# Performance work log

Hardware: AMD Instinct MI355X
Metric: run time of the kernel (lower is better)

The kernel has to match this reference:

```python
import jax, jax.numpy as jnp
import numpy as np

B, T, D_IN, D_MODEL, K = 32, 2048, 512, 1024, 64


def setup_inputs() -> dict:
    key = jax.random.key(0)
    ks = jax.random.split(key, 13)

    def lin(k, fan_in, fan_out):
        kw, kb = jax.random.split(k)
        bound = 1.0 / np.sqrt(fan_in)
        W = jax.random.uniform(kw, (fan_in, fan_out), minval=-bound, maxval=bound, dtype=jnp.float32)
        b = jax.random.uniform(kb, (fan_out,), minval=-bound, maxval=bound, dtype=jnp.float32)
        return W, b

    x = jax.random.normal(ks[0], (B, T, D_IN), dtype=jnp.float32)
    W_theta, b_theta = lin(ks[1], D_IN, K)
    W_lam, b_lam = lin(ks[2], D_IN, D_MODEL)
    W_delt, b_delt = lin(ks[3], D_IN, D_MODEL)
    W_inp, b_inp = lin(ks[4], D_IN, D_MODEL)
    W_par, b_par = lin(ks[5], 2 * K, 2)
    W_add, b_add = lin(ks[6], D_MODEL, 1)
    return {
        "x": x,
        "W_theta": W_theta, "b_theta": b_theta,
        "W_lam": W_lam, "b_lam": b_lam,
        "W_delt": W_delt, "b_delt": b_delt,
        "W_inp": W_inp, "b_inp": b_inp,
        "W_par": W_par, "b_par": b_par,
        "W_add": W_add, "b_add": b_add,
    }


def _forward(x, W_theta, b_theta, W_lam, b_lam, W_delt, b_delt, W_inp, b_inp, W_par, b_par, W_add, b_add):
    # Rotation recurrence: g starts at (1, 0) and is multiplied by e^{i*th_t} each
    # step, so the final g is exactly e^{i * sum_t th_t} (angles compose additively).
    th = jnp.pi * (jnp.einsum('btd,dk->btk', x, W_theta) + b_theta)  # (B,T,K)
    ang = jnp.sum(th, axis=1)                                        # (B,K)
    g_feat = jnp.concatenate([jnp.cos(ang), jnp.sin(ang)], axis=-1)  # (B,2K)

    # SSM state recurrence: s_t = alpha_t * s_{t-1} + delt_t * inp_t
    lam = jax.nn.softplus(jnp.einsum('btd,dm->btm', x, W_lam) + b_lam)
    delt = jax.nn.softplus(jnp.einsum('btd,dm->btm', x, W_delt) + b_delt)
    inp = jnp.einsum('btd,dm->btm', x, W_inp) + b_inp
    alpha = jnp.exp(-delt * lam)          # (B,T,M)
    drive = delt * inp                    # (B,T,M)

    def step(s, ad):
        a, d = ad
        return a * s + d, None

    s0 = jnp.zeros((x.shape[0], W_lam.shape[1]), dtype=x.dtype)
    s, _ = jax.lax.scan(step, s0, (jnp.swapaxes(alpha, 0, 1), jnp.swapaxes(drive, 0, 1)))

    parity_logits = g_feat @ W_par + b_par  # (B,2)
    add_pred = s @ W_add + b_add            # (B,1)
    return parity_logits, add_pred


def reference(x, W_theta, b_theta, W_lam, b_lam, W_delt, b_delt, W_inp, b_inp, W_par, b_par, W_add, b_add):
    return _forward(x, W_theta, b_theta, W_lam, b_lam, W_delt, b_delt, W_inp, b_inp, W_par, b_par, W_add, b_add)
```

## Files before the change

### kernel.cpp

```cpp
#include <hip/hip_runtime.h>
#include <hip/hip_bf16.h>

#define B_   32
#define T_   2048
#define DIN  512
#define DM   1024
#define K_   64
#define BT   64
#define NC   (T_/BT)
#define MT   (DM/64)
#define LDSTR 68

typedef unsigned short u16;
typedef unsigned int   u32;

__device__ __forceinline__ float bf2f(u16 h) {
    return __uint_as_float(((u32)h) << 16);
}
__device__ __forceinline__ void bf2x2(u32 w, float& lo, float& hi) {
    lo = __uint_as_float(w << 16);
    hi = __uint_as_float(w & 0xffff0000u);
}
__device__ __forceinline__ u16 f2bf(float f) {
    u32 u = __float_as_uint(f);
    u += 0x7fffu + ((u >> 16) & 1u);
    return (u16)(u >> 16);
}
__device__ __forceinline__ float softplusf(float z) {
    return fmaxf(z, 0.0f) + log1pf(expf(-fabsf(z)));
}

template<bool BF16>
__device__ __forceinline__ float ld1(const void* p, size_t i) {
    if (BF16) return bf2f(((const u16*)p)[i]);
    else      return ((const float*)p)[i];
}
template<bool BF16>
__device__ __forceinline__ void ld2(const void* p, size_t i, float& a, float& b) {
    if (BF16) { u32 w = *(const u32*)((const u16*)p + i); bf2x2(w, a, b); }
    else      { float2 v = *(const float2*)((const float*)p + i); a = v.x; b = v.y; }
}
template<bool BF16>
__device__ __forceinline__ void ld8(const void* p, size_t i, float* a) {
    if (BF16) {
        uint4 v = *(const uint4*)((const u16*)p + i);
        bf2x2(v.x, a[0], a[1]); bf2x2(v.y, a[2], a[3]);
        bf2x2(v.z, a[4], a[5]); bf2x2(v.w, a[6], a[7]);
    } else {
        float4 v0 = *(const float4*)((const float*)p + i);
        float4 v1 = *(const float4*)((const float*)p + i + 4);
        a[0]=v0.x; a[1]=v0.y; a[2]=v0.z; a[3]=v0.w;
        a[4]=v1.x; a[5]=v1.y; a[6]=v1.z; a[7]=v1.w;
    }
}

__device__ __forceinline__ bool sniff_is_bf16(const void* xraw) {
    __shared__ int flag_s;
    if (threadIdx.x < 64) {
        u16 w = ((const u16*)xraw)[threadIdx.x];
        float av = fabsf(bf2f(w));
        bool plausible = (av == 0.0f) || (av >= 9.094947e-13f && av <= 64.0f);
        unsigned long long m = __ballot(plausible ? 1 : 0);
        if (threadIdx.x == 0) flag_s = (__popcll(m) >= 56) ? 1 : 0;
    }
    __syncthreads();
    return flag_s != 0;
}

__global__ __launch_bounds__(64) void zero_accum_kernel(const void* x, void* out) {
    bool isbf = sniff_is_bf16(x);
    float* outf = (float*)out;
    if (threadIdx.x < 32) {
        if (isbf) outf[threadIdx.x] = 0.0f;
        else      outf[64 + threadIdx.x] = 0.0f;
    }
}

typedef __attribute__((ext_vector_type(8)))  short bf16x8;
typedef __attribute__((ext_vector_type(16))) float f32x16;

#define TCH 128
#define NCH (T_/TCH)
#define A_OFF  0
#define W_OFF  16384
#define AL_OFF 0
#define DR_OFF 32768

#define WS_COL_FLOATS  16384
#define WS_W_OFF_F     16384
#define WS_W_PLANE_U32 (3*256*1024)
#define WS_WFRAG_OFF_B 65536ULL
#define WS_WFRAG_BYTES (16ULL*16*24*1024)
#define WS_XFRAG_OFF_B (WS_WFRAG_OFF_B + WS_WFRAG_BYTES)
#define WS_XFRAG_BYTES (32ULL*16*16*16*1024)
#define WS_FULL_BYTES  (WS_XFRAG_OFF_B + WS_XFRAG_BYTES)

#define KC  64
__global__ __launch_bounds__(256, 2) void fused_ssm_mfma_bf16(
    const void* __restrict__ x,
    const void* __restrict__ Wlam, const void* __restrict__ blam,
    const void* __restrict__ Wdelt, const void* __restrict__ bdelt,
    const void* __restrict__ Winp, const void* __restrict__ binp,
    const void* __restrict__ Wadd,
    void* __restrict__ out)
{
    __shared__ __align__(16) unsigned char LDS[65536];

    const int tid = threadIdx.x;

    {
        int* flag = (int*)LDS;
        if (tid < 64) {
            u16 w0 = ((const u16*)x)[tid];
            float av = fabsf(bf2f(w0));
            bool plausible = (av == 0.0f) || (av >= 9.094947e-13f && av <= 64.0f);
            unsigned long long m = __ballot(plausible ? 1 : 0);
            if (tid == 0) *flag = (__popcll(m) >= 56) ? 1 : 0;
        }
        __syncthreads();
        int isbf = *flag;
        __syncthreads();
        if (!isbf) return;
    }

    const int swz = (blockIdx.x & 7) * 64 + (blockIdx.x >> 3);
    const int mg  = swz & 15;
    const int b   = swz >> 4;
    const int m0  = mg * 64;

    const int lane = tid & 63;
    const int w    = tid >> 6;
    const int p    = w >> 1;
    const int h    = w & 1;
    const int lr   = lane & 31;
    const int lg   = lane >> 5;

    const int colg = m0 + h*32 + lr;
    const float bL = bf2f(((const u16*)blam )[colg]);
    const float bD = bf2f(((const u16*)bdelt)[colg]);
    const float bI = bf2f(((const u16*)binp )[colg]);

    float* alphaS = (float*)(LDS + AL_OFF);
    float* driveS = (float*)(LDS + DR_OFF);

    float scarry = 0.0f;

    #pragma unroll 1
    for (int c = 0; c < NCH; c++) {
        f32x16 aL0, aL1, aD0, aD1, aI0, aI1;
        #pragma unroll
        for (int r = 0; r < 16; r++) {
            aL0[r] = bL; aL1[r] = bL;
            aD0[r] = bD; aD1[r] = bD;
            aI0[r] = bI; aI1[r] = bI;
        }

        #pragma unroll 1
        for (int kc = 0; kc < DIN/KC; kc++) {
            {
                const int t_l  = tid >> 1;
                const int half = tid & 1;
                const u16* xp = (const u16*)x
                    + ((size_t)b*T_ + (size_t)c*TCH + t_l)*DIN + kc*KC + half*32;
                uint4 v[4];
                v[0] = *(const uint4*)(xp);
                v[1] = *(const uint4*)(xp + 8);
                v[2] = *(const uint4*)(xp + 16);
                v[3] = *(const uint4*)(xp + 24);
                const int tt = t_l >> 5, tr = t_l & 31;
                #pragma unroll
                for (int q = 0; q < 4; q++) {
                    const int o  = half*4 + q;
                    const int ks = o >> 1, g = o & 1;
                    *(uint4*)(LDS + A_OFF + ((tt*4 + ks) << 10) + ((g*32 + tr) << 4)) = v[q];
                }
            }
            #pragma unroll
            for (int i = 0; i < 6; i++) {
                const int f   = w + 4*i;
                const int nt  = f >> 2, ks = f & 3;
                const int hh  = (nt >= 3) ? 1 : 0;
                const int mat = nt - 3*hh;
                const u16* Wp = (const u16*)(mat == 0 ? Wlam : (mat == 1 ? Wdelt : Winp));
                const size_t base = (size_t)(kc*KC + ks*16 + lg*8)*DM + (size_t)(m0 + hh*32 + lr);
                u32 e0 = Wp[base        ];
                u32 e1 = Wp[base +   DM ];
                u32 e2 = Wp[base + 2*DM ];
                u32 e3 = Wp[base + 3*DM ];
                u32 e4 = Wp[base + 4*DM ];
                u32 e5 = Wp[base + 5*DM ];
                u32 e6 = Wp[base + 6*DM ];
                u32 e7 = Wp[base + 7*DM ];
                uint4 pk;
                pk.x = e0 | (e1 << 16);
                pk.y = e2 | (e3 << 16);
                pk.z = e4 | (e5 << 16);
                pk.w = e6 | (e7 << 16);
                *(uint4*)(LDS + W_OFF + (f << 10) + (lane << 4)) = pk;
            }
            __syncthreads();

            #pragma unroll
            for (int ks = 0; ks < 4; ks++) {
                bf16x8 a0 = *(const bf16x8*)(LDS + A_OFF + (((2*p    )*4 + ks) << 10) + (lane << 4));
                bf16x8 a1 = *(const bf16x8*)(LDS + A_OFF + (((2*p + 1)*4 + ks) << 10) + (lane << 4));
                bf16x8 vL = *(const bf16x8*)(LDS + W_OFF + (((h*3 + 0)*4 + ks) << 10) + (lane << 4));
                bf16x8 vD = *(const bf16x8*)(LDS + W_OFF + (((h*3 + 1)*4 + ks) << 10) + (lane << 4));
                bf16x8 vI = *(const bf16x8*)(LDS + W_OFF + (((h*3 + 2)*4 + ks) << 10) + (lane << 4));
                aL0 = __builtin_amdgcn_mfma_f32_32x32x16_bf16(a0, vL, aL0, 0, 0, 0);
                aL1 = __builtin_amdgcn_mfma_f32_32x32x16_bf16(a1, vL, aL1, 0, 0, 0);
                aD0 = __builtin_amdgcn_mfma_f32_32x32x16_bf16(a0, vD, aD0, 0, 0, 0);
                aD1 = __builtin_amdgcn_mfma_f32_32x32x16_bf16(a1, vD, aD1, 0, 0, 0);
                aI0 = __builtin_amdgcn_mfma_f32_32x32x16_bf16(a0, vI, aI0, 0, 0, 0);
                aI1 = __builtin_amdgcn_mfma_f32_32x32x16_bf16(a1, vI, aI1, 0, 0, 0);
            }
            __syncthreads();
        }

        #pragma unroll
        for (int tt2 = 0; tt2 < 2; tt2++) {
            #pragma unroll
            for (int r = 0; r < 16; r++) {
                const float zl = tt2 ? aL1[r] : aL0[r];
                const float zd = tt2 ? aD1[r] : aD0[r];
                const float zi = tt2 ? aI1[r] : aI0[r];
                const float lam = softplusf(zl);
                const float dl  = softplusf(zd);
                const float av  = expf(-dl * lam);
                const float dv  = dl * zi;
                const int t_loc = (2*p + tt2)*32 + (r & 3) + 8*(r >> 2) + 4*lg;
                const int m_loc = h*32 + lr;
                alphaS[t_loc*64 + m_loc] = av;
                driveS[t_loc*64 + m_loc] = dv;
            }
        }
        __syncthreads();

        if (tid < 64) {
            float s = scarry;
            #pragma unroll 8
            for (int t = 0; t < TCH; t++)
                s = fmaf(alphaS[t*64 + tid], s, driveS[t*64 + tid]);
            scarry = s;
        }
        __syncthreads();
    }

    if (tid < 64) {
        float partial = scarry * bf2f(((const u16*)Wadd)[m0 + tid]);
        #pragma unroll
        for (int off = 32; off > 0; off >>= 1)
            partial += __shfl_down(partial, off, 64);
        if (tid == 0)
            atomicAdd(&((float*)out)[b], partial);
    }
}

__global__ __launch_bounds__(256) void convert_w_kernel(
    const void* __restrict__ x,
    const void* __restrict__ Wlam, const void* __restrict__ Wdelt,
    const void* __restrict__ Winp, float* __restrict__ ws)
{
    if (sniff_is_bf16(x)) return;
    const int mat = blockIdx.x >> 8;
    const int kp  = blockIdx.x & 255;
    const float* Wp = (mat == 0) ? (const float*)Wlam
                    : (mat == 1) ? (const float*)Wdelt : (const float*)Winp;
    u32* whi = (u32*)(ws + WS_W_OFF_F);
    u32* wlo = whi + WS_W_PLANE_U32;
    const size_t ro = (size_t)(2*kp)*DM;
    const size_t wo = ((size_t)mat*256 + kp)*DM;
    #pragma unroll
    for (int mm = 0; mm < 4; mm++) {
        const int m = mm*256 + threadIdx.x;
        float a0 = Wp[ro + m];
        float a1 = Wp[ro + DM + m];
        u16 h0 = f2bf(a0), h1 = f2bf(a1);
        float l0 = a0 - bf2f(h0);
        float l1 = a1 - bf2f(h1);
        whi[wo + m] = (u32)h0 | ((u32)h1 << 16);
        wlo[wo + m] = (__float_as_uint(l0) >> 16) | (__float_as_uint(l1) & 0xffff0000u);
    }
}

__global__ __launch_bounds__(256) void convert_w_frag_kernel(
    const void* __restrict__ x,
    const void* __restrict__ Wlam, const void* __restrict__ Wdelt,
    const void* __restrict__ Winp, u32* __restrict__ wsw)
{
    if (sniff_is_bf16(x)) return;
    const int kc = blockIdx.x & 15;
    const int mg = blockIdx.x >> 4;
    const int m0 = mg*64;
    u32* dst = wsw + (size_t)(mg*16 + kc) * 6144;
    #pragma unroll
    for (int i = 0; i < 6; i++) {
        const int u = threadIdx.x + 256*i;
        const int f = u >> 6;
        const int l = u & 63;
        const int hl = f & 1, ks = (f >> 1) & 1, nt = f >> 2;
        const int hh = nt / 3, mat = nt % 3;
        const float* Wp = (mat == 0) ? (const float*)Wlam
                        : (mat == 1) ? (const float*)Wdelt : (const float*)Winp;
        const int lr = l & 31, lg = l >> 5;
        const int kp0 = kc*16 + ks*8 + lg*4;
        const int m = m0 + hh*32 + lr;
        u32 q4[4];
        #pragma unroll
        for (int q = 0; q < 4; q++) {
            float a0 = Wp[(size_t)(2*(kp0+q)    )*DM + m];
            float a1 = Wp[(size_t)(2*(kp0+q) + 1)*DM + m];
            u16 h0 = f2bf(a0), h1 = f2bf(a1);
            if (hl == 0) {
                q4[q] = (u32)h0 | ((u32)h1 << 16);
            } else {
                float l0 = a0 - bf2f(h0);
                float l1 = a1 - bf2f(h1);
                q4[q] = (__float_as_uint(l0) >> 16) | (__float_as_uint(l1) & 0xffff0000u);
            }
        }
        *(uint4*)(dst + f*256 + l*4) = make_uint4(q4[0], q4[1], q4[2], q4[3]);
    }
}

#define KC2 32
__global__ __launch_bounds__(256) void convert_x_kernel(
    const void* __restrict__ x, u32* __restrict__ wsx)
{
    if (sniff_is_bf16(x)) return;
    const int kc = blockIdx.x & 15;
    const int c  = (blockIdx.x >> 4) & 15;
    const int b  = blockIdx.x >> 8;
    const int tid = threadIdx.x;
    const int t_l  = tid >> 1;
    const int half = tid & 1;
    const float* xp = (const float*)x
        + ((size_t)b*T_ + (size_t)c*TCH + t_l)*DIN + kc*KC2 + half*16;
    float vv[16];
    *(float4*)(vv)      = *(const float4*)(xp);
    *(float4*)(vv + 4)  = *(const float4*)(xp + 4);
    *(float4*)(vv + 8)  = *(const float4*)(xp + 8);
    *(float4*)(vv + 12) = *(const float4*)(xp + 12);
    u32 hi[8], lo[8];
    #pragma unroll
    for (int q = 0; q < 8; q++) {
        const float a0 = vv[2*q], a1 = vv[2*q+1];
        const u16 h0 = f2bf(a0), h1 = f2bf(a1);
        hi[q] = (u32)h0 | ((u32)h1 << 16);
        const float l0 = a0 - bf2f(h0);
        const float l1 = a1 - bf2f(h1);
        lo[q] = (__float_as_uint(l0) >> 16) | (__float_as_uint(l1) & 0xffff0000u);
    }
    u32* dst = wsx + ((((size_t)b*16 + c)*16 + kc) << 12);
    const int tt = t_l >> 5, tr = t_l & 31;
    const int fb = (tt*2 + half)*2;
    *(uint4*)(dst + fb*256     + (0*32 + tr)*4) = make_uint4(hi[0],hi[1],hi[2],hi[3]);
    *(uint4*)(dst + fb*256     + (1*32 + tr)*4) = make_uint4(hi[4],hi[5],hi[6],hi[7]);
    *(uint4*)(dst + (fb+1)*256 + (0*32 + tr)*4) = make_uint4(lo[0],lo[1],lo[2],lo[3]);
    *(uint4*)(dst + (fb+1)*256 + (1*32 + tr)*4) = make_uint4(lo[4],lo[5],lo[6],lo[7]);
}

#define STG_B 40960
__global__ __launch_bounds__(256, 2) void fused_ssm_mfma_fp32_full(
    const void* __restrict__ x,
    const void* __restrict__ blam, const void* __restrict__ bdelt,
    const void* __restrict__ binp, const void* __restrict__ Wadd,
    const u32* __restrict__ wsw, const u32* __restrict__ wsx,
    void* __restrict__ out)
{
    __shared__ __align__(16) unsigned char LDS[2*STG_B];

    const int tid = threadIdx.x;

    {
        int* flag = (int*)LDS;
        if (tid < 64) {
            u16 w0 = ((const u16*)x)[tid];
            float av = fabsf(bf2f(w0));
            bool plausible = (av == 0.0f) || (av >= 9.094947e-13f && av <= 64.0f);
            unsigned long long m = __ballot(plausible ? 1 : 0);
            if (tid == 0) *flag = (__popcll(m) >= 56) ? 1 : 0;
        }
        __syncthreads();
        int isbf = *flag;
        __syncthreads();
        if (isbf) return;
    }

    const int swz = (blockIdx.x & 7) * 64 + (blockIdx.x >> 3);
    const int mg  = swz & 15;
    const int b   = swz >> 4;
    const int m0  = mg * 64;

    const int lane = tid & 63;
    const int w    = tid >> 6;
    const int p    = w >> 1;
    const int h    = w & 1;
    const int lr   = lane & 31;
    const int lg   = lane >> 5;

    const int colg = m0 + h*32 + lr;
    const float bL = ((const float*)blam )[colg];
    const float bD = ((const float*)bdelt)[colg];
    const float bI = ((const float*)binp )[colg];

    float* alphaS = (float*)(LDS + AL_OFF);
    float* driveS = (float*)(LDS + DR_OFF);

    float scarry = 0.0f;

    #pragma unroll 1
    for (int c = 0; c < NCH; c++) {
        f32x16 aL0, aL1, aD0, aD1, aI0, aI1;
        #pragma unroll
        for (int r = 0; r < 16; r++) {
            aL0[r] = bL; aL1[r] = bL;
            aD0[r] = bD; aD1[r] = bD;
            aI0[r] = bI; aI1[r] = bI;
        }

        {
            const u32* ga = wsx + ((((size_t)b*16 + c)*16 + 0) << 12);
            const u32* gw = wsw + (size_t)(mg*16 + 0)*6144;
            uint4 sa[4], sw[6];
            #pragma unroll
            for (int j = 0; j < 4; j++) sa[j] = *(const uint4*)(ga + ((size_t)tid + 256*j)*4);
            #pragma unroll
            for (int j = 0; j < 6; j++) sw[j] = *(const uint4*)(gw + ((size_t)tid + 256*j)*4);
            #pragma unroll
            for (int j = 0; j < 4; j++) *(uint4*)(LDS + ((tid + 256*j) << 4)) = sa[j];
            #pragma unroll
            for (int j = 0; j < 6; j++) *(uint4*)(LDS + 16384 + ((tid + 256*j) << 4)) = sw[j];
        }
        __syncthreads();

        #pragma unroll 1
        for (int kc = 0; kc < DIN/KC2; kc++) {
            unsigned char* cur = LDS + (kc & 1)*STG_B;

            if (kc < DIN/KC2 - 1) {
                unsigned char* nxt = LDS + ((kc + 1) & 1)*STG_B;
                const u32* ga = wsx + ((((size_t)b*16 + c)*16 + (kc+1)) << 12);
                const u32* gw = wsw + (size_t)(mg*16 + (kc+1))*6144;
                uint4 sa[4], sw[6];
                #pragma unroll
                for (int j = 0; j < 4; j++) sa[j] = *(const uint4*)(ga + ((size_t)tid + 256*j)*4);
                #pragma unroll
                for (int j = 0; j < 6; j++) sw[j] = *(const uint4*)(gw + ((size_t)tid + 256*j)*4);
                #pragma unroll
                for (int j = 0; j < 4; j++) *(uint4*)(nxt + ((tid + 256*j) << 4)) = sa[j];
                #pragma unroll
                for (int j = 0; j < 6; j++) *(uint4*)(nxt + 16384 + ((tid + 256*j) << 4)) = sw[j];
            }

            #pragma unroll
            for (int ks = 0; ks < 2; ks++) {
                const int fa0 = ((2*p    )*2 + ks)*2;
                const int fa1 = ((2*p + 1)*2 + ks)*2;
                const int fL  = ((h*3 + 0)*2 + ks)*2;
                const int fD  = ((h*3 + 1)*2 + ks)*2;
                const int fI  = ((h*3 + 2)*2 + ks)*2;
                bf16x8 a0h = *(const bf16x8*)(cur + (fa0     << 10) + (lane << 4));
                bf16x8 a0l = *(const bf16x8*)(cur + ((fa0+1) << 10) + (lane << 4));
                bf16x8 a1h = *(const bf16x8*)(cur + (fa1     << 10) + (lane << 4));
                bf16x8 a1l = *(const bf16x8*)(cur + ((fa1+1) << 10) + (lane << 4));
                bf16x8 vLh = *(const bf16x8*)(cur + 16384 + (fL      << 10) + (lane << 4));
                bf16x8 vLl = *(const bf16x8*)(cur + 16384 + ((fL+1)  << 10) + (lane << 4));
                bf16x8 vDh = *(const bf16x8*)(cur + 16384 + (fD      << 10) + (lane << 4));
                bf16x8 vDl = *(const bf16x8*)(cur + 16384 + ((fD+1)  << 10) + (lane << 4));
                bf16x8 vIh = *(const bf16x8*)(cur + 16384 + (fI      << 10) + (lane << 4));
                bf16x8 vIl = *(const bf16x8*)(cur + 16384 + ((fI+1)  << 10) + (lane << 4));
                aL0 = __builtin_amdgcn_mfma_f32_32x32x16_bf16(a0h, vLh, aL0, 0, 0, 0);
                aL0 = __builtin_amdgcn_mfma_f32_32x32x16_bf16(a0h, vLl, aL0, 0, 0, 0);
                aL0 = __builtin_amdgcn_mfma_f32_32x32x16_bf16(a0l, vLh, aL0, 0, 0, 0);
                aL1 = __builtin_amdgcn_mfma_f32_32x32x16_bf16(a1h, vLh, aL1, 0, 0, 0);
                aL1 = __builtin_amdgcn_mfma_f32_32x32x16_bf16(a1h, vLl, aL1, 0, 0, 0);
                aL1 = __builtin_amdgcn_mfma_f32_32x32x16_bf16(a1l, vLh, aL1, 0, 0, 0);
                aD0 = __builtin_amdgcn_mfma_f32_32x32x16_bf16(a0h, vDh, aD0, 0, 0, 0);
                aD0 = __builtin_amdgcn_mfma_f32_32x32x16_bf16(a0h, vDl, aD0, 0, 0, 0);
                aD0 = __builtin_amdgcn_mfma_f32_32x32x16_bf16(a0l, vDh, aD0, 0, 0, 0);
                aD1 = __builtin_amdgcn_mfma_f32_32x32x16_bf16(a1h, vDh, aD1, 0, 0, 0);
                aD1 = __builtin_amdgcn_mfma_f32_32x32x16_bf16(a1h, vDl, aD1, 0, 0, 0);
                aD1 = __builtin_amdgcn_mfma_f32_32x32x16_bf16(a1l, vDh, aD1, 0, 0, 0);
                aI0 = __builtin_amdgcn_mfma_f32_32x32x16_bf16(a0h, vIh, aI0, 0, 0, 0);
                aI0 = __builtin_amdgcn_mfma_f32_32x32x16_bf16(a0h, vIl, aI0, 0, 0, 0);
                aI0 = __builtin_amdgcn_mfma_f32_32x32x16_bf16(a0l, vIh, aI0, 0, 0, 0);
                aI1 = __builtin_amdgcn_mfma_f32_32x32x16_bf16(a1h, vIh, aI1, 0, 0, 0);
                aI1 = __builtin_amdgcn_mfma_f32_32x32x16_bf16(a1h, vIl, aI1, 0, 0, 0);
                aI1 = __builtin_amdgcn_mfma_f32_32x32x16_bf16(a1l, vIh, aI1, 0, 0, 0);
            }
            __syncthreads();
        }

        #pragma unroll
        for (int tt2 = 0; tt2 < 2; tt2++) {
            #pragma unroll
            for (int r = 0; r < 16; r++) {
                const float zl = tt2 ? aL1[r] : aL0[r];
                const float zd = tt2 ? aD1[r] : aD0[r];
                const float zi = tt2 ? aI1[r] : aI0[r];
                const float lam = softplusf(zl);
                const float dl  = softplusf(zd);
                const float av  = expf(-dl * lam);
                const float dv  = dl * zi;
                const int t_loc = (2*p + tt2)*32 + (r & 3) + 8*(r >> 2) + 4*lg;
                const int m_loc = h*32 + lr;
                alphaS[t_loc*64 + m_loc] = av;
                driveS[t_loc*64 + m_loc] = dv;
            }
        }
        __syncthreads();

        if (tid < 64) {
            float s = scarry;
            #pragma unroll 8
            for (int t = 0; t < TCH; t++)
                s = fmaf(alphaS[t*64 + tid], s, driveS[t*64 + tid]);
            scarry = s;
        }
        __syncthreads();
    }

    if (tid < 64) {
        float partial = scarry * ((const float*)Wadd)[m0 + tid];
        #pragma unroll
        for (int off = 32; off > 0; off >>= 1)
            partial += __shfl_down(partial, off, 64);
        if (tid == 0)
            atomicAdd(&((float*)out)[64 + b], partial);
    }
}

__global__ __launch_bounds__(256, 2) void fused_ssm_mfma_fp32_ws6(
    const void* __restrict__ x,
    const void* __restrict__ blam, const void* __restrict__ bdelt,
    const void* __restrict__ binp, const void* __restrict__ Wadd,
    const float* __restrict__ ws,
    void* __restrict__ out)
{
    __shared__ __align__(16) unsigned char LDS[65536];

    const int tid = threadIdx.x;

    {
        int* flag = (int*)LDS;
        if (tid < 64) {
            u16 w0 = ((const u16*)x)[tid];
            float av = fabsf(bf2f(w0));
            bool plausible = (av == 0.0f) || (av >= 9.094947e-13f && av <= 64.0f);
            unsigned long long m = __ballot(plausible ? 1 : 0);
            if (tid == 0) *flag = (__popcll(m) >= 56) ? 1 : 0;
        }
        __syncthreads();
        int isbf = *flag;
        __syncthreads();
        if (isbf) return;
    }

    const u32* whi = (const u32*)(ws + WS_W_OFF_F);
    const u32* wlo = whi + WS_W_PLANE_U32;

    const int swz = (blockIdx.x & 7) * 64 + (blockIdx.x >> 3);
    const int mg  = swz & 15;
    const int b   = swz >> 4;
    const int m0  = mg * 64;

    const int lane = tid & 63;
    const int w    = tid >> 6;
    const int p    = w >> 1;
    const int h    = w & 1;
    const int lr   = lane & 31;
    const int lg   = lane >> 5;

    const int colg = m0 + h*32 + lr;
    const float bL = ((const float*)blam )[colg];
    const float bD = ((const float*)bdelt)[colg];
    const float bI = ((const float*)binp )[colg];

    int fhi_[3], kp0_[3]; size_t wb_[3];
    #pragma unroll
    for (int i = 0; i < 3; i++) {
        const int u2 = w + 4*i;
        const int ks = u2 & 1, mu = u2 >> 1;
        const int mat = mu % 3, hh = mu / 3;
        fhi_[i] = 2*u2;
        kp0_[i] = ks*8 + lg*4;
        wb_[i]  = ((size_t)mat*256)*DM + (size_t)(m0 + hh*32 + lr);
    }

    float* alphaS = (float*)(LDS + AL_OFF);
    float* driveS = (float*)(LDS + DR_OFF);

    float scarry = 0.0f;

    #pragma unroll 1
    for (int c = 0; c < NCH; c++) {
        f32x16 aL0, aL1, aD0, aD1, aI0, aI1;
        #pragma unroll
        for (int r = 0; r < 16; r++) {
            aL0[r] = bL; aL1[r] = bL;
            aD0[r] = bD; aD1[r] = bD;
            aI0[r] = bI; aI1[r] = bI;
        }

        #pragma unroll 1
        for (int kc = 0; kc < DIN/KC2; kc++) {
            {
                const int t_l  = tid >> 1;
                const int half = tid & 1;
                const float* xp = (const float*)x
                    + ((size_t)b*T_ + (size_t)c*TCH + t_l)*DIN + kc*KC2 + half*16;
                float vv[16];
                *(float4*)(vv)      = *(const float4*)(xp);
                *(float4*)(vv + 4)  = *(const float4*)(xp + 4);
                *(float4*)(vv + 8)  = *(const float4*)(xp + 8);
                *(float4*)(vv + 12) = *(const float4*)(xp + 12);
                u32 hi[8], lo[8];
                #pragma unroll
                for (int q = 0; q < 8; q++) {
                    const float a0 = vv[2*q], a1 = vv[2*q+1];
                    const u16 h0 = f2bf(a0), h1 = f2bf(a1);
                    hi[q] = (u32)h0 | ((u32)h1 << 16);
                    const float l0 = a0 - bf2f(h0);
                    const float l1 = a1 - bf2f(h1);
                    lo[q] = (__float_as_uint(l0) >> 16) | (__float_as_uint(l1) & 0xffff0000u);
                }
                const int tt = t_l >> 5, tr = t_l & 31;
                const int fb = (tt*2 + half)*2;
                *(uint4*)(LDS + A_OFF + (fb << 10)     + ((0*32 + tr) << 4)) = make_uint4(hi[0],hi[1],hi[2],hi[3]);
                *(uint4*)(LDS + A_OFF + (fb << 10)     + ((1*32 + tr) << 4)) = make_uint4(hi[4],hi[5],hi[6],hi[7]);
                *(uint4*)(LDS + A_OFF + ((fb+1) << 10) + ((0*32 + tr) << 4)) = make_uint4(lo[0],lo[1],lo[2],lo[3]);
                *(uint4*)(LDS + A_OFF + ((fb+1) << 10) + ((1*32 + tr) << 4)) = make_uint4(lo[4],lo[5],lo[6],lo[7]);
            }
            #pragma unroll
            for (int i = 0; i < 3; i++) {
                const size_t base = wb_[i] + (size_t)(kc*16 + kp0_[i])*DM;
                uint4 ph, pl;
                ph.x = whi[base]; ph.y = whi[base + DM]; ph.z = whi[base + 2*DM]; ph.w = whi[base + 3*DM];
                pl.x = wlo[base]; pl.y = wlo[base + DM]; pl.z = wlo[base + 2*DM]; pl.w = wlo[base + 3*DM];
                *(uint4*)(LDS + W_OFF + (fhi_[i] << 10)       + (lane << 4)) = ph;
                *(uint4*)(LDS + W_OFF + ((fhi_[i] + 1) << 10) + (lane << 4)) = pl;
            }
            __syncthreads();

            #pragma unroll
            for (int ks = 0; ks < 2; ks++) {
                const int fa0 = ((2*p    )*2 + ks)*2;
                const int fa1 = ((2*p + 1)*2 + ks)*2;
                const int fL  = ((h*3 + 0)*2 + ks)*2;
                const int fD  = ((h*3 + 1)*2 + ks)*2;
                const int fI  = ((h*3 + 2)*2 + ks)*2;
                bf16x8 a0h = *(const bf16x8*)(LDS + A_OFF + (fa0     << 10) + (lane << 4));
                bf16x8 a0l = *(const bf16x8*)(LDS + A_OFF + ((fa0+1) << 10) + (lane << 4));
                bf16x8 a1h = *(const bf16x8*)(LDS + A_OFF + (fa1     << 10) + (lane << 4));
                bf16x8 a1l = *(const bf16x8*)(LDS + A_OFF + ((fa1+1) << 10) + (lane << 4));
                bf16x8 vLh = *(const bf16x8*)(LDS + W_OFF + (fL      << 10) + (lane << 4));
                bf16x8 vLl = *(const bf16x8*)(LDS + W_OFF + ((fL+1)  << 10) + (lane << 4));
                bf16x8 vDh = *(const bf16x8*)(LDS + W_OFF + (fD      << 10) + (lane << 4));
                bf16x8 vDl = *(const bf16x8*)(LDS + W_OFF + ((fD+1)  << 10) + (lane << 4));
                bf16x8 vIh = *(const bf16x8*)(LDS + W_OFF + (fI      << 10) + (lane << 4));
                bf16x8 vIl = *(const bf16x8*)(LDS + W_OFF + ((fI+1)  << 10) + (lane << 4));
                aL0 = __builtin_amdgcn_mfma_f32_32x32x16_bf16(a0h, vLh, aL0, 0, 0, 0);
                aL0 = __builtin_amdgcn_mfma_f32_32x32x16_bf16(a0h, vLl, aL0, 0, 0, 0);
                aL0 = __builtin_amdgcn_mfma_f32_32x32x16_bf16(a0l, vLh, aL0, 0, 0, 0);
                aL1 = __builtin_amdgcn_mfma_f32_32x32x16_bf16(a1h, vLh, aL1, 0, 0, 0);
                aL1 = __builtin_amdgcn_mfma_f32_32x32x16_bf16(a1h, vLl, aL1, 0, 0, 0);
                aL1 = __builtin_amdgcn_mfma_f32_32x32x16_bf16(a1l, vLh, aL1, 0, 0, 0);
                aD0 = __builtin_amdgcn_mfma_f32_32x32x16_bf16(a0h, vDh, aD0, 0, 0, 0);
                aD0 = __builtin_amdgcn_mfma_f32_32x32x16_bf16(a0h, vDl, aD0, 0, 0, 0);
                aD0 = __builtin_amdgcn_mfma_f32_32x32x16_bf16(a0l, vDh, aD0, 0, 0, 0);
                aD1 = __builtin_amdgcn_mfma_f32_32x32x16_bf16(a1h, vDh, aD1, 0, 0, 0);
                aD1 = __builtin_amdgcn_mfma_f32_32x32x16_bf16(a1h, vDl, aD1, 0, 0, 0);
                aD1 = __builtin_amdgcn_mfma_f32_32x32x16_bf16(a1l, vDh, aD1, 0, 0, 0);
                aI0 = __builtin_amdgcn_mfma_f32_32x32x16_bf16(a0h, vIh, aI0, 0, 0, 0);
                aI0 = __builtin_amdgcn_mfma_f32_32x32x16_bf16(a0h, vIl, aI0, 0, 0, 0);
                aI0 = __builtin_amdgcn_mfma_f32_32x32x16_bf16(a0l, vIh, aI0, 0, 0, 0);
                aI1 = __builtin_amdgcn_mfma_f32_32x32x16_bf16(a1h, vIh, aI1, 0, 0, 0);
                aI1 = __builtin_amdgcn_mfma_f32_32x32x16_bf16(a1h, vIl, aI1, 0, 0, 0);
                aI1 = __builtin_amdgcn_mfma_f32_32x32x16_bf16(a1l, vIh, aI1, 0, 0, 0);
            }
            __syncthreads();
        }

        #pragma unroll
        for (int tt2 = 0; tt2 < 2; tt2++) {
            #pragma unroll
            for (int r = 0; r < 16; r++) {
                const float zl = tt2 ? aL1[r] : aL0[r];
                const float zd = tt2 ? aD1[r] : aD0[r];
                const float zi = tt2 ? aI1[r] : aI0[r];
                const float lam = softplusf(zl);
                const float dl  = softplusf(zd);
                const float av  = expf(-dl * lam);
                const float dv  = dl * zi;
                const int t_loc = (2*p + tt2)*32 + (r & 3) + 8*(r >> 2) + 4*lg;
                const int m_loc = h*32 + lr;
                alphaS[t_loc*64 + m_loc] = av;
                driveS[t_loc*64 + m_loc] = dv;
            }
        }
        __syncthreads();

        if (tid < 64) {
            float s = scarry;
            #pragma unroll 8
            for (int t = 0; t < TCH; t++)
                s = fmaf(alphaS[t*64 + tid], s, driveS[t*64 + tid]);
            scarry = s;
        }
        __syncthreads();
    }

    if (tid < 64) {
        float partial = scarry * ((const float*)Wadd)[m0 + tid];
        #pragma unroll
        for (int off = 32; off > 0; off >>= 1)
            partial += __shfl_down(partial, off, 64);
        if (tid == 0)
            atomicAdd(&((float*)out)[64 + b], partial);
    }
}

template<bool BF16>
__global__ __launch_bounds__(256) void fused_ssm_kernel(
    const void* __restrict__ x,
    const void* __restrict__ Wlam, const void* __restrict__ blam,
    const void* __restrict__ Wdelt, const void* __restrict__ bdelt,
    const void* __restrict__ Winp, const void* __restrict__ binp,
    const void* __restrict__ Wadd,
    void* __restrict__ out)
{
    if (sniff_is_bf16(x) != BF16) return;

    __shared__ __align__(16) float smem[8704];

    const int mt  = blockIdx.x & 15;
    const int b   = blockIdx.x >> 4;
    const int tid = threadIdx.x;
    const int tx  = tid & 15;
    const int ty  = tid >> 4;

    float bl[4], bd[4], bi[4];
    #pragma unroll
    for (int jj = 0; jj < 4; jj++) {
        int m = mt*64 + tx*4 + jj;
        bl[jj] = ld1<BF16>(blam, m); bd[jj] = ld1<BF16>(bdelt, m); bi[jj] = ld1<BF16>(binp, m);
    }

    float* xsT = smem;
    float* w3  = smem + 32*LDSTR;
    float* alphaS = smem;
    float* driveS = smem + 64*LDSTR;

    const int t_s = tid >> 2;
    const int ko  = (tid & 3) * 8;
    const int wk  = tid >> 3;
    const int wmo = (tid & 7) * 8;

    float scarry = 0.0f;

    for (int c = 0; c < NC; c++) {
        float acc0[4][4], acc1[4][4], acc2[4][4];
        #pragma unroll
        for (int ii = 0; ii < 4; ii++)
            #pragma unroll
            for (int jj = 0; jj < 4; jj++) {
                acc0[ii][jj] = bl[jj]; acc1[ii][jj] = bd[jj]; acc2[ii][jj] = bi[jj];
            }

        const size_t xbase = ((size_t)b*T_ + (size_t)c*BT) * DIN;

        for (int kk0 = 0; kk0 < DIN; kk0 += 32) {
            {
                float a[8];
                ld8<BF16>(x, xbase + (size_t)t_s*DIN + kk0 + ko, a);
                #pragma unroll
                for (int q = 0; q < 8; q++)
                    xsT[(ko + q)*LDSTR + t_s] = a[q];
            }
            #pragma unroll
            for (int mat = 0; mat < 3; mat++) {
                const void* Wp = (mat == 0) ? Wlam : (mat == 1) ? Wdelt : Winp;
                float a[8];
                ld8<BF16>(Wp, (size_t)(kk0 + wk)*DM + mt*64 + wmo, a);
                float* dst = &w3[(mat*32 + wk)*LDSTR + wmo];
                *(float4*)(dst)     = make_float4(a[0],a[1],a[2],a[3]);
                *(float4*)(dst + 4) = make_float4(a[4],a[5],a[6],a[7]);
            }
            __syncthreads();

            #pragma unroll 8
            for (int kkk = 0; kkk < 32; kkk++) {
                float4 xa = *(const float4*)&xsT[kkk*LDSTR + ty*4];
                float4 w0 = *(const float4*)&w3[( 0 + kkk)*LDSTR + tx*4];
                float4 w1 = *(const float4*)&w3[(32 + kkk)*LDSTR + tx*4];
                float4 w2 = *(const float4*)&w3[(64 + kkk)*LDSTR + tx*4];
                float xv[4]  = {xa.x, xa.y, xa.z, xa.w};
                float w0v[4] = {w0.x, w0.y, w0.z, w0.w};
                float w1v[4] = {w1.x, w1.y, w1.z, w1.w};
                float w2v[4] = {w2.x, w2.y, w2.z, w2.w};
                #pragma unroll
                for (int ii = 0; ii < 4; ii++)
                    #pragma unroll
                    for (int jj = 0; jj < 4; jj++) {
                        acc0[ii][jj] = fmaf(xv[ii], w0v[jj], acc0[ii][jj]);
                        acc1[ii][jj] = fmaf(xv[ii], w1v[jj], acc1[ii][jj]);
                        acc2[ii][jj] = fmaf(xv[ii], w2v[jj], acc2[ii][jj]);
                    }
            }
            __syncthreads();
        }

        #pragma unroll
        for (int ii = 0; ii < 4; ii++) {
            int t = ty*4 + ii;
            float a[4], d[4];
            #pragma unroll
            for (int jj = 0; jj < 4; jj++) {
                float lam = softplusf(acc0[ii][jj]);
                float dl  = softplusf(acc1[ii][jj]);
                a[jj] = expf(-dl * lam);
                d[jj] = dl * acc2[ii][jj];
            }
            *(float4*)&alphaS[t*LDSTR + tx*4] = make_float4(a[0],a[1],a[2],a[3]);
            *(float4*)&driveS[t*LDSTR + tx*4] = make_float4(d[0],d[1],d[2],d[3]);
        }
        __syncthreads();

        if (tid < 64) {
            float s = scarry;
            #pragma unroll 8
            for (int t = 0; t < BT; t++)
                s = fmaf(alphaS[t*LDSTR + tid], s, driveS[t*LDSTR + tid]);
            scarry = s;
        }
        __syncthreads();
    }

    if (tid < 64) {
        float partial = scarry * ld1<BF16>(Wadd, mt*64 + tid);
        #pragma unroll
        for (int off = 32; off > 0; off >>= 1)
            partial += __shfl_down(partial, off, 64);
        if (tid == 0) {
            float* outf = (float*)out;
            atomicAdd(BF16 ? &outf[b] : &outf[64 + b], partial);
        }
    }
}

template<bool BF16>
__global__ __launch_bounds__(64) void add_finalize_kernel(
    const void* x, const void* badd, void* out)
{
    if (sniff_is_bf16(x) != BF16) return;
    float bb = ld1<BF16>(badd, 0);
    if (threadIdx.x < 32) {
        float* outf = (float*)out;
        if (BF16) {
            float s = outf[threadIdx.x] + bb;
            ((u16*)out)[64 + threadIdx.x] = f2bf(s);
        } else {
            outf[64 + threadIdx.x] += bb;
        }
    }
}

__global__ __launch_bounds__(256) void colsum_zero_kernel(float* ws) {
    ws[blockIdx.x*256 + threadIdx.x] = 0.0f;
}

template<bool BF16>
__global__ __launch_bounds__(256) void parity_colsum_kernel(
    const void* __restrict__ x, float* __restrict__ ws)
{
    if (sniff_is_bf16(x) != BF16) return;
    const int b  = blockIdx.x >> 3;
    const int sl = blockIdx.x & 7;
    const int tid = threadIdx.x;
    float s0 = 0.0f, s1 = 0.0f;
    const size_t xb = (size_t)b * T_ * DIN;
    for (int t = sl*256; t < (sl+1)*256; t++) {
        float a, c2;
        ld2<BF16>(x, xb + (size_t)t*DIN + 2*tid, a, c2);
        s0 += a; s1 += c2;
    }
    atomicAdd(&ws[b*512 + 2*tid    ], s0);
    atomicAdd(&ws[b*512 + 2*tid + 1], s1);
}

template<bool BF16>
__global__ __launch_bounds__(256) void parity_finish_kernel(
    const void* __restrict__ x, const float* __restrict__ ws,
    const void* __restrict__ Wth, const void* __restrict__ bth,
    const void* __restrict__ Wpar, const void* __restrict__ bpar,
    void* __restrict__ out)
{
    if (sniff_is_bf16(x) != BF16) return;

    __shared__ float xsL[512];
    __shared__ float red[256];
    __shared__ float cosL[64], sinL[64];
    const int b = blockIdx.x;
    const int tid = threadIdx.x;

    xsL[tid]       = ws[b*512 + tid];
    xsL[256 + tid] = ws[b*512 + 256 + tid];
    __syncthreads();

    {
        const int k = tid & 63, seg = tid >> 6;
        float s = 0.0f;
        #pragma unroll 8
        for (int dd = 0; dd < 128; dd++) {
            int d = seg*128 + dd;
            s = fmaf(xsL[d], ld1<BF16>(Wth, (size_t)d*K_ + k), s);
        }
        red[tid] = s;
    }
    __syncthreads();

    if (tid < 64) {
        float s = red[tid] + red[64 + tid] + red[128 + tid] + red[192 + tid];
        float ang = 3.14159265358979323846f * (s + 2048.0f * ld1<BF16>(bth, tid));
        cosL[tid] = cosf(ang);
        sinL[tid] = sinf(ang);
    }
    __syncthreads();

    if (tid < 2) {
        const int j = tid;
        float s = ld1<BF16>(bpar, j);
        for (int k = 0; k < 64; k++) {
            s = fmaf(cosL[k], ld1<BF16>(Wpar, k*2 + j), s);
            s = fmaf(sinL[k], ld1<BF16>(Wpar, (64 + k)*2 + j), s);
        }
        if (BF16) ((u16*)out)[b*2 + j] = f2bf(s);
        else      ((float*)out)[b*2 + j] = s;
    }
}

template<bool BF16>
__global__ __launch_bounds__(256) void parity_kernel(
    const void* __restrict__ x, const void* __restrict__ Wth, const void* __restrict__ bth,
    const void* __restrict__ Wpar, const void* __restrict__ bpar, void* __restrict__ out)
{
    if (sniff_is_bf16(x) != BF16) return;

    __shared__ float xsL[512];
    __shared__ float red[256];
    __shared__ float cosL[64], sinL[64];
    const int b = blockIdx.x;
    const int tid = threadIdx.x;

    {
        float s0 = 0.0f, s1 = 0.0f;
        const size_t xb = (size_t)b * T_ * DIN;
        for (int t = 0; t < T_; t++) {
            float a, c2;
            ld2<BF16>(x, xb + (size_t)t*DIN + 2*tid, a, c2);
            s0 += a; s1 += c2;
        }
        xsL[2*tid] = s0; xsL[2*tid + 1] = s1;
    }
    __syncthreads();

    {
        const int k = tid & 63, seg = tid >> 6;
        float s = 0.0f;
        #pragma unroll 8
        for (int dd = 0; dd < 128; dd++) {
            int d = seg*128 + dd;
            s = fmaf(xsL[d], ld1<BF16>(Wth, (size_t)d*K_ + k), s);
        }
        red[tid] = s;
    }
    __syncthreads();

    if (tid < 64) {
        float s = red[tid] + red[64 + tid] + red[128 + tid] + red[192 + tid];
        float ang = 3.14159265358979323846f * (s + 2048.0f * ld1<BF16>(bth, tid));
        cosL[tid] = cosf(ang);
        sinL[tid] = sinf(ang);
    }
    __syncthreads();

    if (tid < 2) {
        const int j = tid;
        float s = ld1<BF16>(bpar, j);
        for (int k = 0; k < 64; k++) {
            s = fmaf(cosL[k], ld1<BF16>(Wpar, k*2 + j), s);
            s = fmaf(sinL[k], ld1<BF16>(Wpar, (64 + k)*2 + j), s);
        }
        if (BF16) ((u16*)out)[b*2 + j] = f2bf(s);
        else      ((float*)out)[b*2 + j] = s;
    }
}

extern "C" void kernel_launch(void* const* d_in, const int* in_sizes, int n_in,
                              void* d_out, int out_size, void* d_ws, size_t ws_size,
                              hipStream_t stream)
{
    const void* x     = d_in[0];
    const void* Wth   = d_in[1];
    const void* bth   = d_in[2];
    const void* Wlam  = d_in[3];
    const void* blam  = d_in[4];
    const void* Wdelt = d_in[5];
    const void* bdelt = d_in[6];
    const void* Winp  = d_in[7];
    const void* binp  = d_in[8];
    const void* Wpar  = d_in[9];
    const void* bpar  = d_in[10];
    const void* Wadd  = d_in[11];
    const void* badd  = d_in[12];

    const bool ws_col  = ws_size >= (size_t)WS_COL_FLOATS * 4;
    const bool ws_w    = ws_size >= (size_t)WS_W_OFF_F * 4 + (size_t)WS_W_PLANE_U32 * 2 * 4;
    const bool ws_full = ws_size >= (size_t)WS_FULL_BYTES;
    float* ws  = (float*)d_ws;
    u32*   wsw = (u32*)((char*)d_ws + WS_WFRAG_OFF_B);
    u32*   wsx = (u32*)((char*)d_ws + WS_XFRAG_OFF_B);

    zero_accum_kernel<<<1, 64, 0, stream>>>(x, d_out);

    fused_ssm_mfma_bf16<<<B_*16, 256, 0, stream>>>(
        x, Wlam, blam, Wdelt, bdelt, Winp, binp, Wadd, d_out);

    if (ws_full) {
        convert_w_frag_kernel<<<256, 256, 0, stream>>>(x, Wlam, Wdelt, Winp, wsw);
        convert_x_kernel<<<8192, 256, 0, stream>>>(x, wsx);
        fused_ssm_mfma_fp32_full<<<B_*16, 256, 0, stream>>>(
            x, blam, bdelt, binp, Wadd, wsw, wsx, d_out);
    } else if (ws_w) {
        convert_w_kernel<<<768, 256, 0, stream>>>(x, Wlam, Wdelt, Winp, ws);
        fused_ssm_mfma_fp32_ws6<<<B_*16, 256, 0, stream>>>(
            x, blam, bdelt, binp, Wadd, ws, d_out);
    } else {
        fused_ssm_kernel<false><<<B_*MT, 256, 0, stream>>>(
            x, Wlam, blam, Wdelt, bdelt, Winp, binp, Wadd, d_out);
    }

    add_finalize_kernel<true ><<<1, 64, 0, stream>>>(x, badd, d_out);
    add_finalize_kernel<false><<<1, 64, 0, stream>>>(x, badd, d_out);

    if (ws_col) {
        colsum_zero_kernel<<<64, 256, 0, stream>>>(ws);
        parity_colsum_kernel<true ><<<256, 256, 0, stream>>>(x, ws);
        parity_colsum_kernel<false><<<256, 256, 0, stream>>>(x, ws);
        parity_finish_kernel<true ><<<B_, 256, 0, stream>>>(x, ws, Wth, bth, Wpar, bpar, d_out);
        parity_finish_kernel<false><<<B_, 256, 0, stream>>>(x, ws, Wth, bth, Wpar, bpar, d_out);
    } else {
        parity_kernel<true ><<<B_, 256, 0, stream>>>(x, Wth, bth, Wpar, bpar, d_out);
        parity_kernel<false><<<B_, 256, 0, stream>>>(x, Wth, bth, Wpar, bpar, d_out);
    }
}
```

Before: 1.055 ms.

## Load MFMA fragments directly from global memory, dropping LDS double-buffered staging

Removes the LDS double-buffer staging of x and weight fragments in the fused SSM GEMM. Each wave now loads its own pre-swizzled bf16 hi/lo fragments straight from global memory into registers, with no per-k-chunk __syncthreads. This cuts LDS traffic and barrier stalls. The cost is that fragments shared between waves are fetched redundantly from global/L2, and there is no explicit prefetch to hide load latency. The LDS array is still sized 64 KiB for the later alpha/drive stage.

```diff
diff --git a/kernel.cpp b/kernel.cpp
--- a/kernel.cpp
+++ b/kernel.cpp
@@ -360,7 +360,6 @@
     *(uint4*)(dst + (fb+1)*256 + (1*32 + tr)*4) = make_uint4(lo[4],lo[5],lo[6],lo[7]);
 }
 
-#define STG_B 40960
 __global__ __launch_bounds__(256, 2) void fused_ssm_mfma_fp32_full(
     const void* __restrict__ x,
     const void* __restrict__ blam, const void* __restrict__ bdelt,
@@ -368,7 +367,7 @@
     const u32* __restrict__ wsw, const u32* __restrict__ wsx,
     void* __restrict__ out)
 {
-    __shared__ __align__(16) unsigned char LDS[2*STG_B];
+    __shared__ __align__(16) unsigned char LDS[65536];
 
     const int tid = threadIdx.x;
 
@@ -411,94 +410,65 @@
 
     #pragma unroll 1
     for (int c = 0; c < NCH; c++) {
-        f32x16 aL0, aL1, aD0, aD1, aI0, aI1;
-        #pragma unroll
-        for (int r = 0; r < 16; r++) {
-            aL0[r] = bL; aL1[r] = bL;
-            aD0[r] = bD; aD1[r] = bD;
-            aI0[r] = bI; aI1[r] = bI;
-        }
-
-        {
-            const u32* ga = wsx + ((((size_t)b*16 + c)*16 + 0) << 12);
-            const u32* gw = wsw + (size_t)(mg*16 + 0)*6144;
-            uint4 sa[4], sw[6];
-            #pragma unroll
-            for (int j = 0; j < 4; j++) sa[j] = *(const uint4*)(ga + ((size_t)tid + 256*j)*4);
-            #pragma unroll
-            for (int j = 0; j < 6; j++) sw[j] = *(const uint4*)(gw + ((size_t)tid + 256*j)*4);
-            #pragma unroll
-            for (int j = 0; j < 4; j++) *(uint4*)(LDS + ((tid + 256*j) << 4)) = sa[j];
-            #pragma unroll
-            for (int j = 0; j < 6; j++) *(uint4*)(LDS + 16384 + ((tid + 256*j) << 4)) = sw[j];
-        }
-        __syncthreads();
+        f32x16 acc[3][2];
+        #pragma unroll
+        for (int tt2 = 0; tt2 < 2; tt2++)
+            #pragma unroll
+            for (int r = 0; r < 16; r++) {
+                acc[0][tt2][r] = bL;
+                acc[1][tt2][r] = bD;
+                acc[2][tt2][r] = bI;
+            }
+
+        const u32* ga = wsx + ((((size_t)b*16 + c)*16) << 12)
+                            + (size_t)(8*p)*256 + (size_t)lane*4;
+        const u32* gw = wsw + (size_t)(mg*16)*6144
+                            + (size_t)(12*h)*256 + (size_t)lane*4;
 
         #pragma unroll 1
         for (int kc = 0; kc < DIN/KC2; kc++) {
-            unsigned char* cur = LDS + (kc & 1)*STG_B;
-
-            if (kc < DIN/KC2 - 1) {
-                unsigned char* nxt = LDS + ((kc + 1) & 1)*STG_B;
-                const u32* ga = wsx + ((((size_t)b*16 + c)*16 + (kc+1)) << 12);
-                const u32* gw = wsw + (size_t)(mg*16 + (kc+1))*6144;
-                uint4 sa[4], sw[6];
+            bf16x8 A[2][2][2];
+            #pragma unroll
+            for (int tt2 = 0; tt2 < 2; tt2++)
                 #pragma unroll
-                for (int j = 0; j < 4; j++) sa[j] = *(const uint4*)(ga + ((size_t)tid + 256*j)*4);
+                for (int ks = 0; ks < 2; ks++)
+                    #pragma unroll
+                    for (int hl = 0; hl < 2; hl++)
+                        A[tt2][ks][hl] = *(const bf16x8*)(ga + (tt2*4 + ks*2 + hl)*256);
+            bf16x8 Wf[3][2][2];
+            #pragma unroll
+            for (int mat = 0; mat < 3; mat++)
                 #pragma unroll
-                for (int j = 0; j < 6; j++) sw[j] = *(const uint4*)(gw + ((size_t)tid + 256*j)*4);
+                for (int ks = 0; ks < 2; ks++)
+                    #pragma unroll
+                    for (int hl = 0; hl < 2; hl++)
+                        Wf[mat][ks][hl] = *(const bf16x8*)(gw + (mat*4 + ks*2 + hl)*256);
+
+            #pragma unroll
+            for (int ks = 0; ks < 2; ks++)
                 #pragma unroll
-                for (int j = 0; j < 4; j++) *(uint4*)(nxt + ((tid + 256*j) << 4)) = sa[j];
-                #pragma unroll
-                for (int j = 0; j < 6; j++) *(uint4*)(nxt + 16384 + ((tid + 256*j) << 4)) = sw[j];
-            }
-
-            #pragma unroll
-            for (int ks = 0; ks < 2; ks++) {
-                const int fa0 = ((2*p    )*2 + ks)*2;
-                const int fa1 = ((2*p + 1)*2 + ks)*2;
-                const int fL  = ((h*3 + 0)*2 + ks)*2;
-                const int fD  = ((h*3 + 1)*2 + ks)*2;
-                const int fI  = ((h*3 + 2)*2 + ks)*2;
-                bf16x8 a0h = *(const bf16x8*)(cur + (fa0     << 10) + (lane << 4));
-                bf16x8 a0l = *(const bf16x8*)(cur + ((fa0+1) << 10) + (lane << 4));
-                bf16x8 a1h = *(const bf16x8*)(cur + (fa1     << 10) + (lane << 4));
-                bf16x8 a1l = *(const bf16x8*)(cur + ((fa1+1) << 10) + (lane << 4));
-                bf16x8 vLh = *(const bf16x8*)(cur + 16384 + (fL      << 10) + (lane << 4));
-                bf16x8 vLl = *(const bf16x8*)(cur + 16384 + ((fL+1)  << 10) + (lane << 4));
-                bf16x8 vDh = *(const bf16x8*)(cur + 16384 + (fD      << 10) + (lane << 4));
-                bf16x8 vDl = *(const bf16x8*)(cur + 16384 + ((fD+1)  << 10) + (lane << 4));
-                bf16x8 vIh = *(const bf16x8*)(cur + 16384 + (fI      << 10) + (lane << 4));
-                bf16x8 vIl = *(const bf16x8*)(cur + 16384 + ((fI+1)  << 10) + (lane << 4));
-                aL0 = __builtin_amdgcn_mfma_f32_32x32x16_bf16(a0h, vLh, aL0, 0, 0, 0);
-                aL0 = __builtin_amdgcn_mfma_f32_32x32x16_bf16(a0h, vLl, aL0, 0, 0, 0);
-                aL0 = __builtin_amdgcn_mfma_f32_32x32x16_bf16(a0l, vLh, aL0, 0, 0, 0);
-                aL1 = __builtin_amdgcn_mfma_f32_32x32x16_bf16(a1h, vLh, aL1, 0, 0, 0);
-                aL1 = __builtin_amdgcn_mfma_f32_32x32x16_bf16(a1h, vLl, aL1, 0, 0, 0);
-                aL1 = __builtin_amdgcn_mfma_f32_32x32x16_bf16(a1l, vLh, aL1, 0, 0, 0);
-                aD0 = __builtin_amdgcn_mfma_f32_32x32x16_bf16(a0h, vDh, aD0, 0, 0, 0);
-                aD0 = __builtin_amdgcn_mfma_f32_32x32x16_bf16(a0h, vDl, aD0, 0, 0, 0);
-                aD0 = __builtin_amdgcn_mfma_f32_32x32x16_bf16(a0l, vDh, aD0, 0, 0, 0);
-                aD1 = __builtin_amdgcn_mfma_f32_32x32x16_bf16(a1h, vDh, aD1, 0, 0, 0);
-                aD1 = __builtin_amdgcn_mfma_f32_32x32x16_bf16(a1h, vDl, aD1, 0, 0, 0);
-                aD1 = __builtin_amdgcn_mfma_f32_32x32x16_bf16(a1l, vDh, aD1, 0, 0, 0);
-                aI0 = __builtin_amdgcn_mfma_f32_32x32x16_bf16(a0h, vIh, aI0, 0, 0, 0);
-                aI0 = __builtin_amdgcn_mfma_f32_32x32x16_bf16(a0h, vIl, aI0, 0, 0, 0);
-                aI0 = __builtin_amdgcn_mfma_f32_32x32x16_bf16(a0l, vIh, aI0, 0, 0, 0);
-                aI1 = __builtin_amdgcn_mfma_f32_32x32x16_bf16(a1h, vIh, aI1, 0, 0, 0);
-                aI1 = __builtin_amdgcn_mfma_f32_32x32x16_bf16(a1h, vIl, aI1, 0, 0, 0);
-                aI1 = __builtin_amdgcn_mfma_f32_32x32x16_bf16(a1l, vIh, aI1, 0, 0, 0);
-            }
-            __syncthreads();
+                for (int mat = 0; mat < 3; mat++)
+                    #pragma unroll
+                    for (int tt2 = 0; tt2 < 2; tt2++) {
+                        acc[mat][tt2] = __builtin_amdgcn_mfma_f32_32x32x16_bf16(
+                            A[tt2][ks][0], Wf[mat][ks][0], acc[mat][tt2], 0, 0, 0);
+                        acc[mat][tt2] = __builtin_amdgcn_mfma_f32_32x32x16_bf16(
+                            A[tt2][ks][0], Wf[mat][ks][1], acc[mat][tt2], 0, 0, 0);
+                        acc[mat][tt2] = __builtin_amdgcn_mfma_f32_32x32x16_bf16(
+                            A[tt2][ks][1], Wf[mat][ks][0], acc[mat][tt2], 0, 0, 0);
+                    }
+
+            ga += 4096;
+            gw += 6144;
         }
 
         #pragma unroll
         for (int tt2 = 0; tt2 < 2; tt2++) {
             #pragma unroll
             for (int r = 0; r < 16; r++) {
-                const float zl = tt2 ? aL1[r] : aL0[r];
-                const float zd = tt2 ? aD1[r] : aD0[r];
-                const float zi = tt2 ? aI1[r] : aI0[r];
+                const float zl = acc[0][tt2][r];
+                const float zd = acc[1][tt2][r];
+                const float zi = acc[2][tt2][r];
                 const float lam = softplusf(zl);
                 const float dl  = softplusf(zd);
                 const float av  = expf(-dl * lam);
```

New measurement: 1.056 ms. No clear change (+0.0%).
